# Kernel optimization log

Hardware: AMD Instinct MI355X
Metric: run time of the kernel (lower is better)

The kernel has to match this reference:

```python
import jax, jax.numpy as jnp
import numpy as np

BS, C_IN, CTX, TGT = 2, 8, 1024, 96
D_MODEL, N_HEADS, D_FF, N_LAYERS = 256, 16, 1024, 4
PF, SF, PC, SC = 8, 4, 32, 16
NF = (CTX + SF - PF) // SF + 1   # 256 fine patches (incl. end-pad)
NC = (CTX + SC - PC) // SC + 1   # 64 coarse patches
TOTAL = NF + NC                  # 320
EPS = 1e-5
DK = D_MODEL // N_HEADS
SCALE = DK ** -0.5


def _patchify(z, plen, stride):
    # ReplicationPad1d((0, stride)) then unfold -> (bs, c, n_patches, plen)
    pad = jnp.broadcast_to(z[..., -1:], z.shape[:-1] + (stride,))
    zp = jnp.concatenate([z, pad], axis=-1)
    n = (zp.shape[-1] - plen) // stride + 1
    idx = np.arange(n)[:, None] * stride + np.arange(plen)[None, :]
    return zp[..., idx]


def _layernorm(x, s, b):
    m = x.mean(-1, keepdims=True)
    v = jnp.var(x, axis=-1, keepdims=True)
    return (x - m) * jax.lax.rsqrt(v + EPS) * s + b


def setup_inputs() -> dict:
    key = jax.random.key(0)
    ks = jax.random.split(key, 16)
    g = lambda k, shape: jax.random.normal(k, shape, jnp.float32) * 0.02
    return {
        "z": jax.random.normal(ks[0], (BS, C_IN, CTX), jnp.float32),
        "revin_w": jnp.ones((C_IN,), jnp.float32),
        "revin_b": jnp.zeros((C_IN,), jnp.float32),
        "Wf": g(ks[1], (PF, D_MODEL)), "bf": jnp.zeros((D_MODEL,), jnp.float32),
        "Wc": g(ks[2], (PC, D_MODEL)), "bc": jnp.zeros((D_MODEL,), jnp.float32),
        "W_pos": jax.random.uniform(ks[3], (TOTAL, D_MODEL), jnp.float32, -0.02, 0.02),
        "WQ": g(ks[4], (N_LAYERS, D_MODEL, D_MODEL)), "bQ": jnp.zeros((N_LAYERS, D_MODEL), jnp.float32),
        "WK": g(ks[5], (N_LAYERS, D_MODEL, D_MODEL)), "bK": jnp.zeros((N_LAYERS, D_MODEL), jnp.float32),
        "WV": g(ks[6], (N_LAYERS, D_MODEL, D_MODEL)), "bV": jnp.zeros((N_LAYERS, D_MODEL), jnp.float32),
        "WO": g(ks[7], (N_LAYERS, D_MODEL, D_MODEL)), "bO": jnp.zeros((N_LAYERS, D_MODEL), jnp.float32),
        "ln1_s": jnp.ones((N_LAYERS, D_MODEL), jnp.float32), "ln1_b": jnp.zeros((N_LAYERS, D_MODEL), jnp.float32),
        "ln2_s": jnp.ones((N_LAYERS, D_MODEL), jnp.float32), "ln2_b": jnp.zeros((N_LAYERS, D_MODEL), jnp.float32),
        "F1": g(ks[8], (N_LAYERS, D_MODEL, D_FF)), "c1": jnp.zeros((N_LAYERS, D_FF), jnp.float32),
        "F2": g(ks[9], (N_LAYERS, D_FF, D_MODEL)), "c2": jnp.zeros((N_LAYERS, D_MODEL), jnp.float32),
        "Wh": g(ks[10], (D_MODEL * TOTAL, TGT)), "bh": jnp.zeros((TGT,), jnp.float32),
    }


def reference(z, revin_w, revin_b, Wf, bf, Wc, bc, W_pos, WQ, bQ, WK, bK, WV, bV,
              WO, bO, ln1_s, ln1_b, ln2_s, ln2_b, F1, c1, F2, c2, Wh, bh):
    # RevIN norm over the time axis (last axis of (bs, c, T))
    mean = z.mean(-1, keepdims=True)
    std = jnp.sqrt(jnp.var(z, axis=-1, keepdims=True) + EPS)
    zn = (z - mean) / std * revin_w[None, :, None] + revin_b[None, :, None]

    # dual-scale patch embedding
    x_fine = _patchify(zn, PF, SF) @ Wf + bf      # (bs, c, NF, d)
    x_coarse = _patchify(zn, PC, SC) @ Wc + bc    # (bs, c, NC, d)
    x = jnp.concatenate([x_fine, x_coarse], axis=2)  # (bs, c, TOTAL, d)

    u = x.reshape(BS * C_IN, TOTAL, D_MODEL) + W_pos  # (B, S, d), B=bs*c

    # residual-score transformer encoder (post-norm)
    prev = None
    for l in range(N_LAYERS):
        q = (u @ WQ[l] + bQ[l]).reshape(-1, TOTAL, N_HEADS, DK).transpose(0, 2, 1, 3)
        k = (u @ WK[l] + bK[l]).reshape(-1, TOTAL, N_HEADS, DK).transpose(0, 2, 1, 3)
        v = (u @ WV[l] + bV[l]).reshape(-1, TOTAL, N_HEADS, DK).transpose(0, 2, 1, 3)
        s = jnp.einsum('bhqd,bhkd->bhqk', q, k) * SCALE
        if prev is not None:
            s = s + prev
        w = jax.nn.softmax(s, axis=-1)
        o = jnp.einsum('bhqk,bhkd->bhqd', w, v).transpose(0, 2, 1, 3).reshape(-1, TOTAL, D_MODEL)
        o = o @ WO[l] + bO[l]
        u = _layernorm(u + o, ln1_s[l], ln1_b[l])
        h = jax.nn.gelu(u @ F1[l] + c1[l], approximate=False) @ F2[l] + c2[l]
        u = _layernorm(u + h, ln2_s[l], ln2_b[l])
        prev = s

    # head: (bs, c, TOTAL, d) -> permute -> flatten(d, TOTAL) -> linear
    zz = u.reshape(BS, C_IN, TOTAL, D_MODEL).transpose(0, 1, 3, 2).reshape(BS, C_IN, D_MODEL * TOTAL)
    out = zz @ Wh + bh  # (bs, c, TGT)

    # RevIN denorm
    out = (out - revin_b[None, :, None]) / (revin_w[None, :, None] + EPS * EPS) * std + mean
    return out
```

## Files before the change

### kernel.cpp

```cpp
#include <hip/hip_runtime.h>
#include <math.h>

typedef unsigned short ushort;
typedef unsigned int uint;
typedef __attribute__((ext_vector_type(8))) short short8;
typedef __attribute__((ext_vector_type(4))) float f32x4;
typedef __attribute__((ext_vector_type(4))) ushort us4;

constexpr int BS = 2, C_IN = 8, CTX = 1024, TGT = 96;
constexpr int DM = 256, NH = 16, DFF = 1024, NL = 4;
constexpr int NF = 256, TOTAL = 320;
constexpr int NB = 16;
constexpr int DK = 16;
constexpr float EPS = 1e-5f;
constexpr float SCALE = 0.25f;
constexpr int KHEAD = DM * TOTAL;
constexpr int M = NB * TOTAL;

__device__ __forceinline__ ushort f2b(float x) {
    uint u = __float_as_uint(x);
    u += 0x7fff + ((u >> 16) & 1);
    return (ushort)(u >> 16);
}
__device__ __forceinline__ float bu2f(ushort x) { return __uint_as_float(((uint)x) << 16); }
__device__ __forceinline__ uint pack2(float a, float b) { return (uint)f2b(a) | ((uint)f2b(b) << 16); }

typedef __attribute__((address_space(3))) uint lds_u32;
typedef const __attribute__((address_space(1))) uint glb_u32;
__device__ __forceinline__ void ldst16(const void* g, void* l) {
    __builtin_amdgcn_global_load_lds((glb_u32*)g, (lds_u32*)l, 16, 0, 0);
}

#define PIPE_BARRIER() asm volatile("s_waitcnt vmcnt(0)\n\ts_barrier" ::: "memory")

__global__ void k_prep(const float* __restrict__ WQ, const float* __restrict__ WK,
                       const float* __restrict__ WV, const float* __restrict__ WO,
                       const float* __restrict__ F1, const float* __restrict__ F2,
                       const float* __restrict__ Wh,
                       ushort* __restrict__ Wtqkv, ushort* __restrict__ WtO,
                       ushort* __restrict__ Ft1, ushort* __restrict__ Ft2,
                       ushort* __restrict__ WhT2,
                       const float* __restrict__ z, const float* __restrict__ rw,
                       const float* __restrict__ rb, float* __restrict__ zn,
                       const float* __restrict__ bhv, float* __restrict__ outp,
                       float* __restrict__ scalef) {
    __shared__ ushort tile[32][33];
    __shared__ float rr1[16], rr2[16], bcast[2];
    int i = blockIdx.x;
    int tx = threadIdx.x, ty = threadIdx.y;
    if (i < 1024) {
        int zz = i >> 6, w = zz >> 2, l = zz & 3;
        const float* src = (w == 0 ? WQ : (w == 1 ? WK : (w == 2 ? WV : WO))) + l * 65536;
        ushort* dst = (w < 3) ? (Wtqkv + (size_t)l * 768 * 256 + w * 256 * 256)
                              : (WtO + (size_t)l * 65536);
        int c0 = (i & 7) * 32, r0 = ((i >> 3) & 7) * 32;
        tile[ty][tx] = f2b(src[(r0 + ty) * 256 + c0 + tx]);
        __syncthreads();
        dst[(c0 + ty) * 256 + r0 + tx] = tile[tx][ty];
    } else if (i < 2048) {
        int j = i - 1024, l = j >> 8;
        const float* src = F1 + (size_t)l * 262144;
        ushort* dst = Ft1 + (size_t)l * 262144;
        int c0 = (j & 31) * 32, r0 = ((j >> 5) & 7) * 32;
        tile[ty][tx] = f2b(src[(r0 + ty) * 1024 + c0 + tx]);
        __syncthreads();
        dst[(c0 + ty) * 256 + r0 + tx] = tile[tx][ty];
    } else if (i < 3072) {
        int j = i - 2048, l = j >> 8;
        const float* src = F2 + (size_t)l * 262144;
        ushort* dst = Ft2 + (size_t)l * 262144;
        int c0 = (j & 7) * 32, r0 = ((j >> 3) & 31) * 32;
        tile[ty][tx] = f2b(src[(r0 + ty) * 256 + c0 + tx]);
        __syncthreads();
        dst[(c0 + ty) * 1024 + r0 + tx] = tile[tx][ty];
    } else if (i < 10752) {
        int j = i - 3072;
        int t0 = (j % 3) * 32, rest = j / 3;
        int d0 = (rest & 7) * 32, pp = rest >> 3;
        tile[ty][tx] = f2b(Wh[((size_t)(d0 + ty) * 320 + pp) * 96 + t0 + tx]);
        __syncthreads();
        WhT2[(size_t)(t0 + ty) * KHEAD + pp * 256 + d0 + tx] = tile[tx][ty];
    } else {
        int bc = i - 10752;
        int tid = ty * 32 + tx;
        float x = z[bc * CTX + tid];
        float s1 = x, s2 = x * x;
#pragma unroll
        for (int off = 1; off < 64; off <<= 1) {
            s1 += __shfl_xor(s1, off);
            s2 += __shfl_xor(s2, off);
        }
        if ((tid & 63) == 0) { rr1[tid >> 6] = s1; rr2[tid >> 6] = s2; }
        __syncthreads();
        if (tid == 0) {
            float a1 = 0.f, a2 = 0.f;
            for (int k = 0; k < 16; k++) { a1 += rr1[k]; a2 += rr2[k]; }
            float m = a1 * (1.0f / CTX);
            float var = a2 * (1.0f / CTX) - m * m;
            float sd = sqrtf(var + EPS);
            bcast[0] = m; bcast[1] = sd;
        }
        __syncthreads();
        float m = bcast[0], sd = bcast[1];
        int c = bc & 7;
        float w = rw[c], bb = rb[c];
        zn[bc * CTX + tid] = (x - m) / sd * w + bb;
        if (tid < TGT) outp[bc * TGT + tid] = (bhv[tid] - bb) / (w + EPS * EPS) * sd + m;
        if (tid == 0) scalef[bc] = sd / (w + EPS * EPS);
    }
}

__global__ void k_embed(const float* __restrict__ zn, const float* __restrict__ Wf,
                        const float* __restrict__ bfv, const float* __restrict__ Wc,
                        const float* __restrict__ bcv, const float* __restrict__ Wpos,
                        ushort* __restrict__ u) {
    int bc = blockIdx.x / TOTAL, p = blockIdx.x % TOTAL, d = threadIdx.x;
    float acc;
    if (p < NF) {
        acc = bfv[d];
        int base = p * 4;
        for (int i = 0; i < 8; i++) {
            int idx = min(base + i, CTX - 1);
            acc += zn[bc * CTX + idx] * Wf[i * DM + d];
        }
    } else {
        int pc = p - NF;
        acc = bcv[d];
        int base = pc * 16;
        for (int i = 0; i < 32; i++) {
            int idx = min(base + i, CTX - 1);
            acc += zn[bc * CTX + idx] * Wc[i * DM + d];
        }
    }
    acc += Wpos[p * DM + d];
    u[(bc * TOTAL + p) * DM + d] = f2b(acc);
}

template <int GELU, int QKV>
__global__ __launch_bounds__(256) void k_gemm_mfma(const ushort* __restrict__ A,
                                                   const ushort* __restrict__ Wt,
                                                   const float* __restrict__ b0,
                                                   const float* __restrict__ b1,
                                                   const float* __restrict__ b2,
                                                   ushort* __restrict__ C,
                                                   ushort* __restrict__ C2,
                                                   int Mm, int N, int K) {
    __shared__ ushort As[2][64][32];
    __shared__ ushort Bs[2][64][32];
    int tid = threadIdx.x;
    int wave = tid >> 6, lane = tid & 63;
    int quad = lane >> 4, l16 = lane & 15;
    int m0 = blockIdx.y * 64, n0 = blockIdx.x * 64;

    f32x4 acc[4];
#pragma unroll
    for (int nt = 0; nt < 4; nt++) acc[nt] = (f32x4){0.f, 0.f, 0.f, 0.f};

    int srow = wave * 16 + (lane >> 2);
    int sc = (lane & 3) ^ ((srow >> 1) & 3);
    const ushort* Ag = &A[(size_t)(m0 + srow) * K + sc * 8];
    const ushort* Bg = &Wt[(size_t)(n0 + srow) * K + sc * 8];
    int rchunk = (quad ^ ((l16 >> 1) & 3)) * 8;

    ldst16(Ag, &As[0][wave * 16][0]);
    ldst16(Bg, &Bs[0][wave * 16][0]);
    PIPE_BARRIER();

    int nstep = K >> 5;
    int cur = 0;
    for (int t = 0; t < nstep; t++) {
        if (t + 1 < nstep) {
            ldst16(Ag + (t + 1) * 32, &As[cur ^ 1][wave * 16][0]);
            ldst16(Bg + (t + 1) * 32, &Bs[cur ^ 1][wave * 16][0]);
        }
        short8 af = *(const short8*)&As[cur][wave * 16 + l16][rchunk];
#pragma unroll
        for (int nt = 0; nt < 4; nt++) {
            short8 bf = *(const short8*)&Bs[cur][nt * 16 + l16][rchunk];
            acc[nt] = __builtin_amdgcn_mfma_f32_16x16x32_bf16(af, bf, acc[nt], 0, 0, 0);
        }
        PIPE_BARRIER();
        cur ^= 1;
    }
#pragma unroll
    for (int nt = 0; nt < 4; nt++) {
        int col = n0 + nt * 16 + l16;
        float bi;
        if (QKV) {
            int bs = (n0 + nt * 16) >> 8;
            const float* bp = bs == 0 ? b0 : (bs == 1 ? b1 : b2);
            bi = bp[col & 255];
        } else {
            bi = b0[col];
        }
#pragma unroll
        for (int r = 0; r < 4; r++) {
            int rowm = m0 + wave * 16 + quad * 4 + r;
            float vv = acc[nt][r] + bi;
            if (GELU) vv = vv * 0.5f * (1.0f + erff(vv * 0.70710678118f));
            if (QKV) {
                int bs = col >> 8;
                ushort* dst = (bs == 2) ? (C2 + (size_t)rowm * DM)
                                        : (C + (size_t)bs * (M * DM) + (size_t)rowm * DM);
                dst[col & 255] = f2b(vv);
            } else {
                C[(size_t)rowm * N + col] = f2b(vv);
            }
        }
    }
}

__global__ __launch_bounds__(256) void k_gemm_ln16(const ushort* __restrict__ A,
                                                   const ushort* __restrict__ Wt,
                                                   const float* __restrict__ bias,
                                                   const float* __restrict__ ls,
                                                   const float* __restrict__ lb,
                                                   ushort* __restrict__ u, int K) {
    __shared__ ushort As[2][16][32];
    __shared__ ushort Bs[2][256][32];
    __shared__ float ps1[16][4], ps2[16][4];
    int tid = threadIdx.x;
    int wave = tid >> 6, lane = tid & 63;
    int quad = lane >> 4, l16 = lane & 15;
    int m0 = blockIdx.x * 16;

    f32x4 acc[4];
#pragma unroll
    for (int nt = 0; nt < 4; nt++) acc[nt] = (f32x4){0.f, 0.f, 0.f, 0.f};

    int brow = wave * 16 + (lane >> 2);
    int bc_swz = (lane & 3) ^ ((brow >> 1) & 3);
    const ushort* Bg0 = &Wt[(size_t)brow * K + bc_swz * 8];
    int ar = lane >> 2;
    int ac = (lane & 3) ^ ((ar >> 1) & 3);
    const ushort* Ag = &A[(size_t)(m0 + ar) * K + ac * 8];
    int rchunk = (quad ^ ((l16 >> 1) & 3)) * 8;

    if (tid < 64) ldst16(Ag, &As[0][0][0]);
#pragma unroll
    for (int i = 0; i < 4; i++)
        ldst16(Bg0 + (size_t)i * 64 * K, &Bs[0][i * 64 + wave * 16][0]);
    PIPE_BARRIER();

    int nstep = K >> 5;
    int cur = 0;
    for (int t = 0; t < nstep; t++) {
        if (t + 1 < nstep) {
            if (tid < 64) ldst16(Ag + (t + 1) * 32, &As[cur ^ 1][0][0]);
#pragma unroll
            for (int i = 0; i < 4; i++)
                ldst16(Bg0 + (size_t)i * 64 * K + (t + 1) * 32, &Bs[cur ^ 1][i * 64 + wave * 16][0]);
        }
        short8 af = *(const short8*)&As[cur][l16][rchunk];
#pragma unroll
        for (int nt = 0; nt < 4; nt++) {
            short8 bf = *(const short8*)&Bs[cur][wave * 64 + nt * 16 + l16][rchunk];
            acc[nt] = __builtin_amdgcn_mfma_f32_16x16x32_bf16(af, bf, acc[nt], 0, 0, 0);
        }
        PIPE_BARRIER();
        cur ^= 1;
    }
    float xv[4][4];
#pragma unroll
    for (int r = 0; r < 4; r++) {
        int rowg = m0 + quad * 4 + r;
        float s1 = 0.f, s2 = 0.f;
#pragma unroll
        for (int nt = 0; nt < 4; nt++) {
            int col = wave * 64 + nt * 16 + l16;
            float x = acc[nt][r] + bias[col] + bu2f(u[(size_t)rowg * DM + col]);
            xv[r][nt] = x; s1 += x; s2 += x * x;
        }
        s1 += __shfl_xor(s1, 1); s2 += __shfl_xor(s2, 1);
        s1 += __shfl_xor(s1, 2); s2 += __shfl_xor(s2, 2);
        s1 += __shfl_xor(s1, 4); s2 += __shfl_xor(s2, 4);
        s1 += __shfl_xor(s1, 8); s2 += __shfl_xor(s2, 8);
        if (l16 == 0) { ps1[quad * 4 + r][wave] = s1; ps2[quad * 4 + r][wave] = s2; }
    }
    __syncthreads();
#pragma unroll
    for (int r = 0; r < 4; r++) {
        int rowl = quad * 4 + r, rowg = m0 + rowl;
        float s1 = ps1[rowl][0] + ps1[rowl][1] + ps1[rowl][2] + ps1[rowl][3];
        float s2 = ps2[rowl][0] + ps2[rowl][1] + ps2[rowl][2] + ps2[rowl][3];
        float m = s1 * (1.0f / DM);
        float var = s2 * (1.0f / DM) - m * m;
        float rs = rsqrtf(var + EPS);
#pragma unroll
        for (int nt = 0; nt < 4; nt++) {
            int col = wave * 64 + nt * 16 + l16;
            u[(size_t)rowg * DM + col] = f2b((xv[r][nt] - m) * rs * ls[col] + lb[col]);
        }
    }
}

__global__ __launch_bounds__(256, 4) void k_attn(const ushort* __restrict__ qk, const ushort* __restrict__ vm,
                                                 ushort* __restrict__ ao, int nj) {
    __shared__ ushort sh[15360];
    uint* sh32 = (uint*)sh;
    int bh = blockIdx.x, b = bh >> 4, h = bh & 15;
    int i0 = blockIdx.y * 64;
    int t = threadIdx.x, wave = t >> 6, lane = t & 63, quad = lane >> 4, l16 = lane & 15;
    const short8 zero8 = (short8){0, 0, 0, 0, 0, 0, 0, 0};

    f32x4 acc[20];
#pragma unroll
    for (int nt = 0; nt < 20; nt++) acc[nt] = (f32x4){0.f, 0.f, 0.f, 0.f};

    for (int idx = t; idx < 320; idx += 256) {
        int jp = idx >> 1, dh = idx & 1;
        int j = jp * 2;
        uint4 a = *(const uint4*)&vm[((size_t)b * TOTAL + j) * DM + h * DK + dh * 8];
        uint4 bb = *(const uint4*)&vm[((size_t)b * TOTAL + j + 1) * DM + h * DK + dh * 8];
        const ushort* ap = (const ushort*)&a;
        const ushort* bp = (const ushort*)&bb;
        int jr = j & 31;
        int q = (jr & 15) >> 2, jj = ((jr >> 4) << 2) + (jr & 3);
        int base = 10240 + ((j >> 5) * 4 + q) * 128 + jj;
#pragma unroll
        for (int dd = 0; dd < 8; dd++) {
            int d = dh * 8 + dd;
            uint val = (uint)ap[dd] | ((uint)bp[dd] << 16);
            sh32[(base + d * 8) >> 1] = val;
        }
    }

    for (int jl = 0; jl < nj; jl++) {
        const ushort* qm = qk + (size_t)(2 * jl) * M * DM;
        const ushort* km = qm + (size_t)M * DM;
        int kb = (jl & 1) * 5120;
        for (int idx = t; idx < 640; idx += 256) {
            int j = idx >> 1, half = idx & 1;
            short8 kv = *(const short8*)&km[((size_t)b * TOTAL + j) * DM + h * DK + half * 8];
            int jt = j >> 4, jln = j & 15;
            *(short8*)&sh[kb + ((jt * 2 + half) * 16 + jln) * 8] = kv;
        }
        short8 qf = zero8;
        if (quad < 2) qf = *(const short8*)&qm[((size_t)b * TOTAL + i0 + wave * 16 + l16) * DM + h * DK + quad * 8];
        __syncthreads();
#pragma unroll
        for (int nt = 0; nt < 20; nt++) {
            short8 kf = *(const short8*)&sh[kb + ((nt * 2 + (quad & 1)) * 16 + l16) * 8];
            acc[nt] = __builtin_amdgcn_mfma_f32_16x16x32_bf16(kf, qf, acc[nt], 0, 0, 0);
        }
    }

    float mx = -1e30f;
#pragma unroll
    for (int nt = 0; nt < 20; nt++)
#pragma unroll
        for (int r = 0; r < 4; r++) { acc[nt][r] *= SCALE; mx = fmaxf(mx, acc[nt][r]); }
    mx = fmaxf(mx, __shfl_xor(mx, 16));
    mx = fmaxf(mx, __shfl_xor(mx, 32));
    float sum = 0.f;
#pragma unroll
    for (int nt = 0; nt < 20; nt++)
#pragma unroll
        for (int r = 0; r < 4; r++) { acc[nt][r] = __expf(acc[nt][r] - mx); sum += acc[nt][r]; }
    sum += __shfl_xor(sum, 16);
    sum += __shfl_xor(sum, 32);
    float inv = 1.f / sum;
#pragma unroll
    for (int nt = 0; nt < 20; nt++)
#pragma unroll
        for (int r = 0; r < 4; r++) acc[nt][r] *= inv;

    f32x4 oacc = (f32x4){0.f, 0.f, 0.f, 0.f};
#pragma unroll
    for (int jt2 = 0; jt2 < 10; jt2++) {
        short8 vt = *(const short8*)&sh[10240 + ((jt2 * 4 + quad) * 16 + l16) * 8];
        union { short8 v; uint u[4]; } pf;
        pf.u[0] = pack2(acc[2 * jt2][0], acc[2 * jt2][1]);
        pf.u[1] = pack2(acc[2 * jt2][2], acc[2 * jt2][3]);
        pf.u[2] = pack2(acc[2 * jt2 + 1][0], acc[2 * jt2 + 1][1]);
        pf.u[3] = pack2(acc[2 * jt2 + 1][2], acc[2 * jt2 + 1][3]);
        oacc = __builtin_amdgcn_mfma_f32_16x16x32_bf16(vt, pf.v, oacc, 0, 0, 0);
    }
    us4 ov4 = (us4){f2b(oacc[0]), f2b(oacc[1]), f2b(oacc[2]), f2b(oacc[3])};
    *(us4*)&ao[((size_t)b * TOTAL + i0 + wave * 16 + l16) * DM + h * DK + quad * 4] = ov4;
}

__global__ __launch_bounds__(256) void k_head(const ushort* __restrict__ u, const ushort* __restrict__ WhT2,
                                              const float* __restrict__ scalef, float* __restrict__ out) {
    int t0 = blockIdx.x * 16;
    int wave = threadIdx.x >> 6, lane = threadIdx.x & 63;
    int quad = lane >> 4, l16 = lane & 15;
    int chunk = blockIdx.y * 4 + wave;
    int kbeg = chunk * 1024;
    f32x4 acc = (f32x4){0.f, 0.f, 0.f, 0.f};
    const ushort* za = &u[(size_t)l16 * KHEAD + quad * 8];
    const ushort* wb = &WhT2[(size_t)(t0 + l16) * KHEAD + quad * 8];
#pragma unroll 4
    for (int k = kbeg; k < kbeg + 1024; k += 32) {
        short8 af = *(const short8*)&za[k];
        short8 bf = *(const short8*)&wb[k];
        acc = __builtin_amdgcn_mfma_f32_16x16x32_bf16(af, bf, acc, 0, 0, 0);
    }
#pragma unroll
    for (int r = 0; r < 4; r++) {
        int bcr = quad * 4 + r;
        atomicAdd(&out[bcr * TGT + t0 + l16], acc[r] * scalef[bcr]);
    }
}

extern "C" void kernel_launch(void* const* d_in, const int* in_sizes, int n_in,
                              void* d_out, int out_size, void* d_ws, size_t ws_size,
                              hipStream_t stream) {
    const float* z       = (const float*)d_in[0];
    const float* revin_w = (const float*)d_in[1];
    const float* revin_b = (const float*)d_in[2];
    const float* Wf      = (const float*)d_in[3];
    const float* bfv     = (const float*)d_in[4];
    const float* Wc      = (const float*)d_in[5];
    const float* bcv     = (const float*)d_in[6];
    const float* Wpos    = (const float*)d_in[7];
    const float* WQ      = (const float*)d_in[8];
    const float* bQ      = (const float*)d_in[9];
    const float* WK      = (const float*)d_in[10];
    const float* bK      = (const float*)d_in[11];
    const float* WV      = (const float*)d_in[12];
    const float* bV      = (const float*)d_in[13];
    const float* WO      = (const float*)d_in[14];
    const float* bO      = (const float*)d_in[15];
    const float* ln1s    = (const float*)d_in[16];
    const float* ln1b    = (const float*)d_in[17];
    const float* ln2s    = (const float*)d_in[18];
    const float* ln2b    = (const float*)d_in[19];
    const float* F1      = (const float*)d_in[20];
    const float* c1      = (const float*)d_in[21];
    const float* F2      = (const float*)d_in[22];
    const float* c2      = (const float*)d_in[23];
    const float* Wh      = (const float*)d_in[24];
    const float* bh      = (const float*)d_in[25];
    float* out = (float*)d_out;

    char* p = (char*)d_ws;
    float* scalef = (float*)p;   p += 16 * 4;
    p = (char*)(((size_t)p + 255) & ~255ull);
    float* zn = (float*)p;       p += NB * CTX * 4;
    ushort* u     = (ushort*)p;  p += (size_t)M * DM * 2;
    ushort* qkbuf = (ushort*)p;  p += (size_t)NL * 2 * M * DM * 2;
    ushort* vbuf  = (ushort*)p;  p += (size_t)M * DM * 2;
    ushort* ax    = (ushort*)p;  p += (size_t)M * DM * 2;
    ushort* hbuf  = (ushort*)p;  p += (size_t)M * DFF * 2;
    ushort* Wtqkv = (ushort*)p;  p += (size_t)NL * 768 * 256 * 2;
    ushort* WtO   = (ushort*)p;  p += (size_t)NL * 256 * 256 * 2;
    ushort* Ft1   = (ushort*)p;  p += (size_t)NL * 1024 * 256 * 2;
    ushort* Ft2   = (ushort*)p;  p += (size_t)NL * 256 * 1024 * 2;
    ushort* WhT2  = (ushort*)p;  p += (size_t)TGT * KHEAD * 2;

    k_prep<<<10768, dim3(32, 32), 0, stream>>>(WQ, WK, WV, WO, F1, F2, Wh,
                                               Wtqkv, WtO, Ft1, Ft2, WhT2,
                                               z, revin_w, revin_b, zn,
                                               bh, out, scalef);
    k_embed<<<NB * TOTAL, 256, 0, stream>>>(zn, Wf, bfv, Wc, bcv, Wpos, u);

    for (int l = 0; l < NL; l++) {
        k_gemm_mfma<0, 1><<<dim3(12, 80), 256, 0, stream>>>(
            u, Wtqkv + (size_t)l * 768 * 256, bQ + l * DM, bK + l * DM, bV + l * DM,
            qkbuf + (size_t)l * 2 * M * DM, vbuf, M, 768, 256);
        k_attn<<<dim3(NB * NH, 5), 256, 0, stream>>>(qkbuf, vbuf, ax, l + 1);
        k_gemm_ln16<<<M / 16, 256, 0, stream>>>(
            ax, WtO + (size_t)l * 65536, bO + l * DM, ln1s + l * DM, ln1b + l * DM, u, 256);
        k_gemm_mfma<1, 0><<<dim3(16, 80), 256, 0, stream>>>(
            u, Ft1 + (size_t)l * 262144, c1 + l * DFF, c1, c1, hbuf, hbuf, M, 1024, 256);
        k_gemm_ln16<<<M / 16, 256, 0, stream>>>(
            hbuf, Ft2 + (size_t)l * 262144, c2 + l * DM, ln2s + l * DM, ln2b + l * DM, u, 1024);
    }

    k_head<<<dim3(TGT / 16, 20), 256, 0, stream>>>(u, WhT2, scalef, out);
}
```

Baseline: 460.3 us.

## Fuse patch embedding into prep kernel and vectorize weight transposes

Folds the separate embedding kernel into the prep kernel. Each block recomputes the RevIN statistics for one series, keeps the normalized series in LDS, and embeds four patches, so the zn global buffer and one launch go away. The weight-transpose paths switch from 32x32 tiles with 1024-thread blocks to 64-wide tiles with float4 loads and 4-element bf16 stores, cutting the block count from about 10.7k to 3.3k. The cost is redundant per-block mean/variance reductions over the same series (80 blocks each) and heavier per-thread work in the embed blocks.

```diff
diff --git a/kernel.cpp b/kernel.cpp
--- a/kernel.cpp
+++ b/kernel.cpp
@@ -33,107 +33,132 @@
 
 #define PIPE_BARRIER() asm volatile("s_waitcnt vmcnt(0)\n\ts_barrier" ::: "memory")
 
-__global__ void k_prep(const float* __restrict__ WQ, const float* __restrict__ WK,
-                       const float* __restrict__ WV, const float* __restrict__ WO,
-                       const float* __restrict__ F1, const float* __restrict__ F2,
-                       const float* __restrict__ Wh,
-                       ushort* __restrict__ Wtqkv, ushort* __restrict__ WtO,
-                       ushort* __restrict__ Ft1, ushort* __restrict__ Ft2,
-                       ushort* __restrict__ WhT2,
-                       const float* __restrict__ z, const float* __restrict__ rw,
-                       const float* __restrict__ rb, float* __restrict__ zn,
-                       const float* __restrict__ bhv, float* __restrict__ outp,
-                       float* __restrict__ scalef) {
-    __shared__ ushort tile[32][33];
-    __shared__ float rr1[16], rr2[16], bcast[2];
-    int i = blockIdx.x;
-    int tx = threadIdx.x, ty = threadIdx.y;
-    if (i < 1024) {
-        int zz = i >> 6, w = zz >> 2, l = zz & 3;
-        const float* src = (w == 0 ? WQ : (w == 1 ? WK : (w == 2 ? WV : WO))) + l * 65536;
-        ushort* dst = (w < 3) ? (Wtqkv + (size_t)l * 768 * 256 + w * 256 * 256)
-                              : (WtO + (size_t)l * 65536);
-        int c0 = (i & 7) * 32, r0 = ((i >> 3) & 7) * 32;
-        tile[ty][tx] = f2b(src[(r0 + ty) * 256 + c0 + tx]);
+__global__ __launch_bounds__(256) void k_prep(
+        const float* __restrict__ WQ, const float* __restrict__ WK,
+        const float* __restrict__ WV, const float* __restrict__ WO,
+        const float* __restrict__ F1, const float* __restrict__ F2,
+        const float* __restrict__ Wh,
+        ushort* __restrict__ Wtqkv, ushort* __restrict__ WtO,
+        ushort* __restrict__ Ft1, ushort* __restrict__ Ft2,
+        ushort* __restrict__ WhT2,
+        const float* __restrict__ z, const float* __restrict__ rw,
+        const float* __restrict__ rb,
+        const float* __restrict__ Wf, const float* __restrict__ bfv,
+        const float* __restrict__ Wc, const float* __restrict__ bcv,
+        const float* __restrict__ Wpos, ushort* __restrict__ u,
+        const float* __restrict__ bhv, float* __restrict__ outp,
+        float* __restrict__ scalef) {
+    __shared__ __align__(16) ushort tile[64 * 98];
+    __shared__ float szn[CTX];
+    __shared__ float red1[4], red2[4];
+    int i = blockIdx.x, tid = threadIdx.x;
+
+    if (i < 768) {
+        const float* src; ushort* dst; int lsrc, ldst_, r0, c0;
+        if (i < 256) {
+            int mat = i >> 4, l = mat >> 2, w = mat & 3;
+            src = (w == 0 ? WQ : (w == 1 ? WK : (w == 2 ? WV : WO))) + l * 65536;
+            dst = (w < 3) ? (Wtqkv + (size_t)l * 768 * 256 + w * 65536)
+                          : (WtO + (size_t)l * 65536);
+            lsrc = 256; ldst_ = 256; r0 = ((i >> 2) & 3) * 64; c0 = (i & 3) * 64;
+        } else if (i < 512) {
+            int j = i - 256, l = j >> 6, t = j & 63;
+            src = F1 + (size_t)l * 262144; dst = Ft1 + (size_t)l * 262144;
+            lsrc = 1024; ldst_ = 256; r0 = (t >> 4) * 64; c0 = (t & 15) * 64;
+        } else {
+            int j = i - 512, l = j >> 6, t = j & 63;
+            src = F2 + (size_t)l * 262144; dst = Ft2 + (size_t)l * 262144;
+            lsrc = 256; ldst_ = 1024; r0 = (t >> 2) * 64; c0 = (t & 3) * 64;
+        }
+#pragma unroll
+        for (int it = 0; it < 4; it++) {
+            int fid = it * 256 + tid;
+            int fr = fid >> 4, fc = fid & 15;
+            f32x4 v = *(const f32x4*)&src[(size_t)(r0 + fr) * lsrc + c0 + fc * 4];
+            ushort* tr = &tile[fr * 66];
+            tr[fc * 4 + 0] = f2b(v[0]); tr[fc * 4 + 1] = f2b(v[1]);
+            tr[fc * 4 + 2] = f2b(v[2]); tr[fc * 4 + 3] = f2b(v[3]);
+        }
         __syncthreads();
-        dst[(c0 + ty) * 256 + r0 + tx] = tile[tx][ty];
+#pragma unroll
+        for (int it = 0; it < 4; it++) {
+            int sid = it * 256 + tid;
+            int cr = sid >> 4, cc = sid & 15;
+            us4 v = (us4){ tile[(cc * 4 + 0) * 66 + cr], tile[(cc * 4 + 1) * 66 + cr],
+                           tile[(cc * 4 + 2) * 66 + cr], tile[(cc * 4 + 3) * 66 + cr] };
+            *(us4*)&dst[(size_t)(c0 + cr) * ldst_ + r0 + cc * 4] = v;
+        }
     } else if (i < 2048) {
-        int j = i - 1024, l = j >> 8;
-        const float* src = F1 + (size_t)l * 262144;
-        ushort* dst = Ft1 + (size_t)l * 262144;
-        int c0 = (j & 31) * 32, r0 = ((j >> 5) & 7) * 32;
-        tile[ty][tx] = f2b(src[(r0 + ty) * 1024 + c0 + tx]);
+        int j = i - 768;
+        int pp = j >> 2, d0 = (j & 3) * 64;
+#pragma unroll
+        for (int it = 0; it < 6; it++) {
+            int fid = it * 256 + tid;
+            int fr = fid / 24, fc = fid % 24;
+            f32x4 v = *(const f32x4*)&Wh[((size_t)(d0 + fr) * 320 + pp) * 96 + fc * 4];
+            ushort* tr = &tile[fr * 98];
+            tr[fc * 4 + 0] = f2b(v[0]); tr[fc * 4 + 1] = f2b(v[1]);
+            tr[fc * 4 + 2] = f2b(v[2]); tr[fc * 4 + 3] = f2b(v[3]);
+        }
         __syncthreads();
-        dst[(c0 + ty) * 256 + r0 + tx] = tile[tx][ty];
-    } else if (i < 3072) {
-        int j = i - 2048, l = j >> 8;
-        const float* src = F2 + (size_t)l * 262144;
-        ushort* dst = Ft2 + (size_t)l * 262144;
-        int c0 = (j & 7) * 32, r0 = ((j >> 3) & 31) * 32;
-        tile[ty][tx] = f2b(src[(r0 + ty) * 256 + c0 + tx]);
-        __syncthreads();
-        dst[(c0 + ty) * 1024 + r0 + tx] = tile[tx][ty];
-    } else if (i < 10752) {
-        int j = i - 3072;
-        int t0 = (j % 3) * 32, rest = j / 3;
-        int d0 = (rest & 7) * 32, pp = rest >> 3;
-        tile[ty][tx] = f2b(Wh[((size_t)(d0 + ty) * 320 + pp) * 96 + t0 + tx]);
-        __syncthreads();
-        WhT2[(size_t)(t0 + ty) * KHEAD + pp * 256 + d0 + tx] = tile[tx][ty];
+#pragma unroll
+        for (int it = 0; it < 6; it++) {
+            int sid = it * 256 + tid;
+            int tr = sid >> 4, dc = sid & 15;
+            us4 v = (us4){ tile[(dc * 4 + 0) * 98 + tr], tile[(dc * 4 + 1) * 98 + tr],
+                           tile[(dc * 4 + 2) * 98 + tr], tile[(dc * 4 + 3) * 98 + tr] };
+            *(us4*)&WhT2[(size_t)tr * KHEAD + pp * 256 + d0 + dc * 4] = v;
+        }
     } else {
-        int bc = i - 10752;
-        int tid = ty * 32 + tx;
-        float x = z[bc * CTX + tid];
-        float s1 = x, s2 = x * x;
+        int j = i - 2048;
+        int bc = j / 80, pb = j % 80;
+        int wave = tid >> 6, lane = tid & 63;
+        f32x4 zv = *(const f32x4*)&z[bc * CTX + tid * 4];
+        float s1 = zv[0] + zv[1] + zv[2] + zv[3];
+        float s2 = zv[0] * zv[0] + zv[1] * zv[1] + zv[2] * zv[2] + zv[3] * zv[3];
 #pragma unroll
         for (int off = 1; off < 64; off <<= 1) {
             s1 += __shfl_xor(s1, off);
             s2 += __shfl_xor(s2, off);
         }
-        if ((tid & 63) == 0) { rr1[tid >> 6] = s1; rr2[tid >> 6] = s2; }
+        if (lane == 0) { red1[wave] = s1; red2[wave] = s2; }
         __syncthreads();
-        if (tid == 0) {
-            float a1 = 0.f, a2 = 0.f;
-            for (int k = 0; k < 16; k++) { a1 += rr1[k]; a2 += rr2[k]; }
-            float m = a1 * (1.0f / CTX);
-            float var = a2 * (1.0f / CTX) - m * m;
-            float sd = sqrtf(var + EPS);
-            bcast[0] = m; bcast[1] = sd;
-        }
-        __syncthreads();
-        float m = bcast[0], sd = bcast[1];
+        s1 = red1[0] + red1[1] + red1[2] + red1[3];
+        s2 = red2[0] + red2[1] + red2[2] + red2[3];
+        float m = s1 * (1.0f / CTX);
+        float var = s2 * (1.0f / CTX) - m * m;
+        float sd = sqrtf(var + EPS);
         int c = bc & 7;
         float w = rw[c], bb = rb[c];
-        zn[bc * CTX + tid] = (x - m) / sd * w + bb;
-        if (tid < TGT) outp[bc * TGT + tid] = (bhv[tid] - bb) / (w + EPS * EPS) * sd + m;
-        if (tid == 0) scalef[bc] = sd / (w + EPS * EPS);
-    }
-}
-
-__global__ void k_embed(const float* __restrict__ zn, const float* __restrict__ Wf,
-                        const float* __restrict__ bfv, const float* __restrict__ Wc,
-                        const float* __restrict__ bcv, const float* __restrict__ Wpos,
-                        ushort* __restrict__ u) {
-    int bc = blockIdx.x / TOTAL, p = blockIdx.x % TOTAL, d = threadIdx.x;
-    float acc;
-    if (p < NF) {
-        acc = bfv[d];
-        int base = p * 4;
-        for (int i = 0; i < 8; i++) {
-            int idx = min(base + i, CTX - 1);
-            acc += zn[bc * CTX + idx] * Wf[i * DM + d];
-        }
-    } else {
-        int pc = p - NF;
-        acc = bcv[d];
-        int base = pc * 16;
-        for (int i = 0; i < 32; i++) {
-            int idx = min(base + i, CTX - 1);
-            acc += zn[bc * CTX + idx] * Wc[i * DM + d];
-        }
-    }
-    acc += Wpos[p * DM + d];
-    u[(bc * TOTAL + p) * DM + d] = f2b(acc);
+        float inv_sd_w = w / sd;
+#pragma unroll
+        for (int k = 0; k < 4; k++) szn[tid * 4 + k] = (zv[k] - m) * inv_sd_w + bb;
+        if (pb == 0) {
+            if (tid < TGT) outp[bc * TGT + tid] = (bhv[tid] - bb) / (w + EPS * EPS) * sd + m;
+            if (tid == 0) scalef[bc] = sd / (w + EPS * EPS);
+        }
+        __syncthreads();
+#pragma unroll
+        for (int pi = 0; pi < 4; pi++) {
+            int p = pb * 4 + pi, d = tid;
+            float acc;
+            if (p < NF) {
+                acc = bfv[d];
+                int base = p * 4;
+#pragma unroll
+                for (int q = 0; q < 8; q++)
+                    acc += szn[min(base + q, CTX - 1)] * Wf[q * DM + d];
+            } else {
+                acc = bcv[d];
+                int base = (p - NF) * 16;
+#pragma unroll
+                for (int q = 0; q < 32; q++)
+                    acc += szn[min(base + q, CTX - 1)] * Wc[q * DM + d];
+            }
+            acc += Wpos[p * DM + d];
+            u[((size_t)bc * TOTAL + p) * DM + d] = f2b(acc);
+        }
+    }
 }
 
 template <int GELU, int QKV>
@@ -437,7 +462,6 @@
     char* p = (char*)d_ws;
     float* scalef = (float*)p;   p += 16 * 4;
     p = (char*)(((size_t)p + 255) & ~255ull);
-    float* zn = (float*)p;       p += NB * CTX * 4;
     ushort* u     = (ushort*)p;  p += (size_t)M * DM * 2;
     ushort* qkbuf = (ushort*)p;  p += (size_t)NL * 2 * M * DM * 2;
     ushort* vbuf  = (ushort*)p;  p += (size_t)M * DM * 2;
@@ -449,11 +473,11 @@
     ushort* Ft2   = (ushort*)p;  p += (size_t)NL * 256 * 1024 * 2;
     ushort* WhT2  = (ushort*)p;  p += (size_t)TGT * KHEAD * 2;
 
-    k_prep<<<10768, dim3(32, 32), 0, stream>>>(WQ, WK, WV, WO, F1, F2, Wh,
-                                               Wtqkv, WtO, Ft1, Ft2, WhT2,
-                                               z, revin_w, revin_b, zn,
-                                               bh, out, scalef);
-    k_embed<<<NB * TOTAL, 256, 0, stream>>>(zn, Wf, bfv, Wc, bcv, Wpos, u);
+    k_prep<<<3328, 256, 0, stream>>>(WQ, WK, WV, WO, F1, F2, Wh,
+                                     Wtqkv, WtO, Ft1, Ft2, WhT2,
+                                     z, revin_w, revin_b,
+                                     Wf, bfv, Wc, bcv, Wpos, u,
+                                     bh, out, scalef);
 
     for (int l = 0; l < NL; l++) {
         k_gemm_mfma<0, 1><<<dim3(12, 80), 256, 0, stream>>>(
```

After: 441.4 us. -4.1%, faster.
